# Kernel optimization log

Measured on AMD Instinct MI355X. Metric: run time of the kernel, lower is better.

The kernel has to match this reference:

```python
import jax, jax.numpy as jnp
import numpy as np

NUM_CLASSES = 100
CLUSTERS_PER_CLASS = 64
LATENT_DIM = 128
BATCH = 32768


def setup_inputs() -> dict:
    key = jax.random.key(0)
    kx, kc, kl = jax.random.split(key, 3)
    x = jax.random.normal(kx, (BATCH, LATENT_DIM), dtype=jnp.float32)
    # nn.Parameter(torch.randn(C, Kc, D) * 0.1)
    centers = jax.random.normal(kc, (NUM_CLASSES, CLUSTERS_PER_CLASS, LATENT_DIM), dtype=jnp.float32) * 0.1
    labels = jax.random.randint(kl, (BATCH,), 0, NUM_CLASSES, dtype=jnp.int64)
    return {"x": x, "centers": centers, "labels": labels}


def reference(x, centers, labels):
    # [C, Kc, D] -> [K, D]
    all_centers = centers.reshape(-1, LATENT_DIM).astype(x.dtype)
    x2 = jnp.sum(x * x, axis=-1, keepdims=True)            # [B,1]
    c2 = jnp.sum(all_centers * all_centers, axis=-1)       # [K]
    sq = x2 + c2[None, :] - 2.0 * jnp.einsum('bd,kd->bk', x, all_centers)
    distances = jnp.sqrt(jnp.maximum(sq, 0.0))             # [B,K]
    closest_indices = jnp.argmin(distances, axis=1)        # [B]
    class_predictions = closest_indices // CLUSTERS_PER_CLASS
    cluster_assignments = closest_indices % CLUSTERS_PER_CLASS
    quantized_hard = all_centers[closest_indices]          # [B,D]
    min_distances = jnp.take_along_axis(distances, closest_indices[:, None], axis=1)[:, 0]
    # straight-through estimator (training path in the torch module)
    quantized = x + jax.lax.stop_gradient(quantized_hard - x)
    return quantized, cluster_assignments, min_distances, class_predictions
```

## Files before the change

### kernel.cpp

```cpp
#include <hip/hip_runtime.h>
#include <math.h>

#define BATCH  32768
#define D      128
#define K      6400
#define KC     64
#define ROWS_PER_BLOCK 64
#define CHUNK_C 128
#define NCHUNKS 50

typedef _Float16 half8 __attribute__((ext_vector_type(8)));
typedef float    floatx4 __attribute__((ext_vector_type(4)));

typedef __attribute__((address_space(3))) unsigned       lds_uint;
typedef __attribute__((address_space(1))) const unsigned glb_uint;

__device__ __forceinline__ void async_lds16(const void* g, void* l) {
    __builtin_amdgcn_global_load_lds((glb_uint*)g, (lds_uint*)l, 16, 0, 0);
}

__global__ __launch_bounds__(256) void pack_kernel(const float* __restrict__ centers,
                                                   _Float16* __restrict__ wh,
                                                   float* __restrict__ c2n) {
    int tid = blockIdx.x * 256 + threadIdx.x;
    int ch = tid >> 11;
    int u  = (tid >> 7) & 15;
    int cw = tid & 127;
    int center = ch * CHUNK_C + cw;
    const float* src = centers + (size_t)center * D + u * 8;
    float4 a = *(const float4*)src;
    float4 b = *(const float4*)(src + 4);
    float f[8] = {a.x, a.y, a.z, a.w, b.x, b.y, b.z, b.w};
    half8 h;
#pragma unroll
    for (int j = 0; j < 8; ++j) h[j] = (_Float16)f[j];
    *(half8*)(wh + (size_t)tid * 8) = h;

    if (blockIdx.x < K / KC) {
        int c_local = threadIdx.x >> 2, part = threadIdx.x & 3;
        int c = blockIdx.x * 64 + c_local;
        const float4* p = (const float4*)(centers + (size_t)c * D + part * 32);
        float s = 0.f;
#pragma unroll
        for (int i = 0; i < 8; ++i) {
            float4 v = p[i];
            s = fmaf(v.x, v.x, s); s = fmaf(v.y, v.y, s);
            s = fmaf(v.z, v.z, s); s = fmaf(v.w, v.w, s);
        }
        s += __shfl_xor(s, 1, 64);
        s += __shfl_xor(s, 2, 64);
        if (part == 0) c2n[c] = -0.5f * s;
    }
}

__global__ __launch_bounds__(512, 4) void dist_kernel(
    const float* __restrict__ x, const float* __restrict__ centers,
    const _Float16* __restrict__ wh, const float* __restrict__ c2n,
    float* __restrict__ out) {
    __shared__ char lds[65536];

    const int t    = threadIdx.x;
    const int w    = t >> 6;
    const int L    = t & 63;
    const int quad = L >> 4;
    const int n16  = L & 15;
    const int cq   = w & 3;
    const int rq   = w >> 2;
    const int gr0  = blockIdx.x * ROWS_PER_BLOCK;

    half8 Ah[2][4];
#pragma unroll
    for (int rt = 0; rt < 2; ++rt) {
        int r = gr0 + rq * 32 + rt * 16 + n16;
        const float* xr = x + (size_t)r * D + quad * 8;
#pragma unroll
        for (int ks = 0; ks < 4; ++ks) {
            float4 a = *(const float4*)(xr + ks * 32);
            float4 b = *(const float4*)(xr + ks * 32 + 4);
            float f[8] = {a.x, a.y, a.z, a.w, b.x, b.y, b.z, b.w};
            half8 h;
#pragma unroll
            for (int j = 0; j < 8; ++j) h[j] = (_Float16)f[j];
            Ah[rt][ks] = h;
        }
    }

    float b1[8], b2[8];
#pragma unroll
    for (int k = 0; k < 8; ++k) { b1[k] = -1e30f; b2[k] = -1e30f; }

    const char* gh = (const char*)wh;

#pragma unroll
    for (int i = 0; i < 4; ++i) {
        int seg = w + i * 8;
        async_lds16(gh + seg * 1024 + L * 16, lds + seg * 1024);
    }

    float c2vA[2], c2vB[2];
#pragma unroll
    for (int ct = 0; ct < 2; ++ct) c2vA[ct] = c2n[cq * 32 + ct * 16 + n16];
    __syncthreads();

    for (int ci = 0; ci < NCHUNKS; ++ci) {
        const char* cur = lds + (ci & 1) * 32768;
        if (ci + 1 < NCHUNKS) {
            const char* gn = gh + (size_t)(ci + 1) * 32768;
            char* nxt = lds + ((ci + 1) & 1) * 32768;
#pragma unroll
            for (int i = 0; i < 4; ++i) {
                int seg = w + i * 8;
                async_lds16(gn + seg * 1024 + L * 16, nxt + seg * 1024);
            }
            const int kb1 = (ci + 1) * CHUNK_C + cq * 32;
#pragma unroll
            for (int ct = 0; ct < 2; ++ct) c2vB[ct] = c2n[kb1 + ct * 16 + n16];
        }

        floatx4 acc[2][2];
#pragma unroll
        for (int rt = 0; rt < 2; ++rt)
#pragma unroll
            for (int ct = 0; ct < 2; ++ct)
                acc[rt][ct] = (floatx4){c2vA[ct], c2vA[ct], c2vA[ct], c2vA[ct]};

        __builtin_amdgcn_s_setprio(1);
#pragma unroll
        for (int ks = 0; ks < 4; ++ks) {
            const half8* pb = (const half8*)cur + (ks * 4 + quad) * 128 + cq * 32 + n16;
#pragma unroll
            for (int ct = 0; ct < 2; ++ct) {
                half8 Bf = pb[ct * 16];
                acc[0][ct] = __builtin_amdgcn_mfma_f32_16x16x32_f16(Ah[0][ks], Bf, acc[0][ct], 0, 0, 0);
                acc[1][ct] = __builtin_amdgcn_mfma_f32_16x16x32_f16(Ah[1][ks], Bf, acc[1][ct], 0, 0, 0);
            }
        }
        __builtin_amdgcn_s_setprio(0);

        const unsigned pk0 = (unsigned)(2 * ci);
        const unsigned pk1 = (unsigned)(2 * ci + 1);
#pragma unroll
        for (int rt = 0; rt < 2; ++rt)
#pragma unroll
            for (int reg = 0; reg < 4; ++reg) {
                int k = rt * 4 + reg;
                float v0 = __uint_as_float((__float_as_uint(acc[rt][0][reg]) & ~127u) | pk0);
                float v1 = __uint_as_float((__float_as_uint(acc[rt][1][reg]) & ~127u) | pk1);
                float v  = fmaxf(v0, v1);
                b2[k] = __builtin_amdgcn_fmed3f(b1[k], b2[k], v);
                b1[k] = fmaxf(b1[k], v);
            }

#pragma unroll
        for (int ct = 0; ct < 2; ++ct) c2vA[ct] = c2vB[ct];

        __syncthreads();
    }

    int* candL = (int*)lds;

#pragma unroll
    for (int k = 0; k < 8; ++k) {
        unsigned u1 = __float_as_uint(b1[k]), u2 = __float_as_uint(b2[k]);
        int e1 = (int)(u1 & 127u), e2 = (int)(u2 & 127u);
        int p1 = (e1 >> 1) * 128 + cq * 32 + (e1 & 1) * 16 + n16;
        int p2 = (e2 >> 1) * 128 + cq * 32 + (e2 & 1) * 16 + n16;
        float v1 = b1[k], v2 = b2[k];
#pragma unroll
        for (int m = 1; m < 16; m <<= 1) {
            float o1 = __shfl_xor(v1, m, 64), o2 = __shfl_xor(v2, m, 64);
            int   q1 = __shfl_xor(p1, m, 64), q2 = __shfl_xor(p2, m, 64);
            bool firstMine = (v1 > o1) || (v1 == o1 && p1 < q1);
            float nv1 = firstMine ? v1 : o1;  int np1 = firstMine ? p1 : q1;
            float cb  = firstMine ? o1 : v1;  int cpi = firstMine ? q1 : p1;
            float ob  = firstMine ? v2 : o2;  int obi = firstMine ? p2 : q2;
            bool secOwn = (ob > cb) || (ob == cb && obi < cpi);
            v1 = nv1; p1 = np1;
            v2 = secOwn ? ob : cb;  p2 = secOwn ? obi : cpi;
        }
        if (n16 == 0) {
            int rloc = rq * 32 + (k >> 2) * 16 + quad * 4 + (k & 3);
            candL[rloc * 8 + cq * 2 + 0] = p1;
            candL[rloc * 8 + cq * 2 + 1] = p2;
        }
    }
    __syncthreads();

    {
        int r = t >> 3, p = t & 7;
        int row = gr0 + r;
        int ix = candL[r * 8 + p];
        const float4* xr4 = (const float4*)(x + (size_t)row * D);
        const float4* c4  = (const float4*)(centers + (size_t)ix * D);
        float dot = 0.f, x2s = 0.f, c2 = 0.f;
#pragma unroll
        for (int d4 = 0; d4 < 32; ++d4) {
            float4 xv = xr4[d4], cv = c4[d4];
            dot = fmaf(xv.x, cv.x, dot); dot = fmaf(xv.y, cv.y, dot);
            dot = fmaf(xv.z, cv.z, dot); dot = fmaf(xv.w, cv.w, dot);
            x2s = fmaf(xv.x, xv.x, x2s); x2s = fmaf(xv.y, xv.y, x2s);
            x2s = fmaf(xv.z, xv.z, x2s); x2s = fmaf(xv.w, xv.w, x2s);
            c2  = fmaf(cv.x, cv.x, c2);  c2  = fmaf(cv.y, cv.y, c2);
            c2  = fmaf(cv.z, cv.z, c2);  c2  = fmaf(cv.w, cv.w, c2);
        }
        float sq = x2s + c2 - 2.f * dot;
#pragma unroll
        for (int m = 1; m < 8; m <<= 1) {
            float osq = __shfl_xor(sq, m, 64);
            int   oix = __shfl_xor(ix, m, 64);
            if (osq < sq || (osq == sq && oix < ix)) { sq = osq; ix = oix; }
        }

        float* out_clu = out + (size_t)BATCH * D;
        float* out_md  = out_clu + BATCH;
        float* out_cls = out_md + BATCH;
        if (p == 0) {
            out_md[row]  = sqrtf(fmaxf(sq, 0.f));
            out_clu[row] = (float)(ix & (KC - 1));
            out_cls[row] = (float)(ix >> 6);
        }

        const float4* cv4 = (const float4*)(centers + (size_t)ix * D) + p * 4;
        const float4* xv4 = (const float4*)(x + (size_t)row * D) + p * 4;
        float4* o4 = (float4*)(out + (size_t)row * D) + p * 4;
#pragma unroll
        for (int i = 0; i < 4; ++i) {
            float4 cv = cv4[i], xv = xv4[i];
            float4 o;
            o.x = xv.x + (cv.x - xv.x);
            o.y = xv.y + (cv.y - xv.y);
            o.z = xv.z + (cv.z - xv.z);
            o.w = xv.w + (cv.w - xv.w);
            o4[i] = o;
        }
    }
}

extern "C" void kernel_launch(void* const* d_in, const int* in_sizes, int n_in,
                              void* d_out, int out_size, void* d_ws, size_t ws_size,
                              hipStream_t stream) {
    const float* x       = (const float*)d_in[0];
    const float* centers = (const float*)d_in[1];
    float* out = (float*)d_out;

    _Float16* wh  = (_Float16*)d_ws;
    float*    c2n = (float*)(wh + (size_t)K * D);

    pack_kernel<<<(K * 16) / 256, 256, 0, stream>>>(centers, wh, c2n);
    dist_kernel<<<BATCH / ROWS_PER_BLOCK, 512, 0, stream>>>(x, centers, wh, c2n, out);
}
```

Measured before the change: 174.5 us.

## Switch to triple-buffered 64-center chunks with one barrier per chunk

Halves the center chunk to 64 entries (16KB) and uses three LDS buffers, prefetching two chunks ahead. The loop now needs only a single s_barrier per chunk, gated by explicit vmcnt waits, and the packing layout and candidate index decode are updated to match. LDS per block drops, which allows raising the occupancy hint from 4 to 6 blocks per CU. In exchange there are twice as many chunk iterations and barriers, and less MFMA work between synchronisations.

Result: slower. 189.7 us (+8.7%).

```diff
diff --git a/kernel.cpp b/kernel.cpp
--- a/kernel.cpp
+++ b/kernel.cpp
@@ -6,8 +6,9 @@
 #define K      6400
 #define KC     64
 #define ROWS_PER_BLOCK 64
-#define CHUNK_C 128
-#define NCHUNKS 50
+#define CHUNK_C 64
+#define NCHUNKS 100
+#define CHUNK_BYTES 16384
 
 typedef _Float16 half8 __attribute__((ext_vector_type(8)));
 typedef float    floatx4 __attribute__((ext_vector_type(4)));
@@ -23,9 +24,9 @@
                                                    _Float16* __restrict__ wh,
                                                    float* __restrict__ c2n) {
     int tid = blockIdx.x * 256 + threadIdx.x;
-    int ch = tid >> 11;
-    int u  = (tid >> 7) & 15;
-    int cw = tid & 127;
+    int ch = tid >> 10;
+    int u  = (tid >> 6) & 15;
+    int cw = tid & 63;
     int center = ch * CHUNK_C + cw;
     const float* src = centers + (size_t)center * D + u * 8;
     float4 a = *(const float4*)src;
@@ -53,11 +54,12 @@
     }
 }
 
-__global__ __launch_bounds__(512, 4) void dist_kernel(
+__global__ __launch_bounds__(512, 6) void dist_kernel(
     const float* __restrict__ x, const float* __restrict__ centers,
     const _Float16* __restrict__ wh, const float* __restrict__ c2n,
     float* __restrict__ out) {
-    __shared__ char lds[65536];
+    __shared__ char bufs[3][CHUNK_BYTES];
+    __shared__ int  candL[ROWS_PER_BLOCK * 8];
 
     const int t    = threadIdx.x;
     const int w    = t >> 6;
@@ -90,81 +92,78 @@
     for (int k = 0; k < 8; ++k) { b1[k] = -1e30f; b2[k] = -1e30f; }
 
     const char* gh = (const char*)wh;
-
-#pragma unroll
-    for (int i = 0; i < 4; ++i) {
+    const int laneoff = cq * 16 + n16;
+
+    char* pA = bufs[0];  char* pB = bufs[1];  char* pC = bufs[2];
+#pragma unroll
+    for (int i = 0; i < 2; ++i) {
         int seg = w + i * 8;
-        async_lds16(gh + seg * 1024 + L * 16, lds + seg * 1024);
-    }
-
-    float c2vA[2], c2vB[2];
-#pragma unroll
-    for (int ct = 0; ct < 2; ++ct) c2vA[ct] = c2n[cq * 32 + ct * 16 + n16];
-    __syncthreads();
+        async_lds16(gh + seg * 1024 + L * 16, pA + seg * 1024);
+    }
+    float c2cur = c2n[laneoff];
+#pragma unroll
+    for (int i = 0; i < 2; ++i) {
+        int seg = w + i * 8;
+        async_lds16(gh + CHUNK_BYTES + seg * 1024 + L * 16, pB + seg * 1024);
+    }
+    float c2nxt = c2n[CHUNK_C + laneoff];
 
     for (int ci = 0; ci < NCHUNKS; ++ci) {
-        const char* cur = lds + (ci & 1) * 32768;
-        if (ci + 1 < NCHUNKS) {
-            const char* gn = gh + (size_t)(ci + 1) * 32768;
-            char* nxt = lds + ((ci + 1) & 1) * 32768;
-#pragma unroll
-            for (int i = 0; i < 4; ++i) {
+        if (ci + 1 < NCHUNKS) { asm volatile("s_waitcnt vmcnt(3)" ::: "memory"); }
+        else                  { asm volatile("s_waitcnt vmcnt(0)" ::: "memory"); }
+        __builtin_amdgcn_sched_barrier(0);
+        __builtin_amdgcn_s_barrier();
+        __builtin_amdgcn_sched_barrier(0);
+
+        floatx4 cinit = (floatx4){c2cur, c2cur, c2cur, c2cur};
+        const half8* pb = (const half8*)pA + quad * 64 + laneoff;
+        floatx4 acc0, acc1;
+        __builtin_amdgcn_s_setprio(1);
+        {
+            half8 Bf = pb[0];
+            acc0 = __builtin_amdgcn_mfma_f32_16x16x32_f16(Ah[0][0], Bf, cinit, 0, 0, 0);
+            acc1 = __builtin_amdgcn_mfma_f32_16x16x32_f16(Ah[1][0], Bf, cinit, 0, 0, 0);
+        }
+#pragma unroll
+        for (int ks = 1; ks < 4; ++ks) {
+            half8 Bf = pb[ks * 256];
+            acc0 = __builtin_amdgcn_mfma_f32_16x16x32_f16(Ah[0][ks], Bf, acc0, 0, 0, 0);
+            acc1 = __builtin_amdgcn_mfma_f32_16x16x32_f16(Ah[1][ks], Bf, acc1, 0, 0, 0);
+        }
+        __builtin_amdgcn_s_setprio(0);
+
+        float c2new = 0.f;
+        if (ci + 2 < NCHUNKS) {
+            const char* gn = gh + (size_t)(ci + 2) * CHUNK_BYTES;
+#pragma unroll
+            for (int i = 0; i < 2; ++i) {
                 int seg = w + i * 8;
-                async_lds16(gn + seg * 1024 + L * 16, nxt + seg * 1024);
+                async_lds16(gn + seg * 1024 + L * 16, pC + seg * 1024);
             }
-            const int kb1 = (ci + 1) * CHUNK_C + cq * 32;
-#pragma unroll
-            for (int ct = 0; ct < 2; ++ct) c2vB[ct] = c2n[kb1 + ct * 16 + n16];
-        }
-
-        floatx4 acc[2][2];
-#pragma unroll
-        for (int rt = 0; rt < 2; ++rt)
-#pragma unroll
-            for (int ct = 0; ct < 2; ++ct)
-                acc[rt][ct] = (floatx4){c2vA[ct], c2vA[ct], c2vA[ct], c2vA[ct]};
-
-        __builtin_amdgcn_s_setprio(1);
-#pragma unroll
-        for (int ks = 0; ks < 4; ++ks) {
-            const half8* pb = (const half8*)cur + (ks * 4 + quad) * 128 + cq * 32 + n16;
-#pragma unroll
-            for (int ct = 0; ct < 2; ++ct) {
-                half8 Bf = pb[ct * 16];
-                acc[0][ct] = __builtin_amdgcn_mfma_f32_16x16x32_f16(Ah[0][ks], Bf, acc[0][ct], 0, 0, 0);
-                acc[1][ct] = __builtin_amdgcn_mfma_f32_16x16x32_f16(Ah[1][ks], Bf, acc[1][ct], 0, 0, 0);
-            }
-        }
-        __builtin_amdgcn_s_setprio(0);
-
-        const unsigned pk0 = (unsigned)(2 * ci);
-        const unsigned pk1 = (unsigned)(2 * ci + 1);
-#pragma unroll
-        for (int rt = 0; rt < 2; ++rt)
-#pragma unroll
-            for (int reg = 0; reg < 4; ++reg) {
-                int k = rt * 4 + reg;
-                float v0 = __uint_as_float((__float_as_uint(acc[rt][0][reg]) & ~127u) | pk0);
-                float v1 = __uint_as_float((__float_as_uint(acc[rt][1][reg]) & ~127u) | pk1);
-                float v  = fmaxf(v0, v1);
-                b2[k] = __builtin_amdgcn_fmed3f(b1[k], b2[k], v);
-                b1[k] = fmaxf(b1[k], v);
-            }
-
-#pragma unroll
-        for (int ct = 0; ct < 2; ++ct) c2vA[ct] = c2vB[ct];
-
-        __syncthreads();
-    }
-
-    int* candL = (int*)lds;
+            c2new = c2n[(ci + 2) * CHUNK_C + laneoff];
+        }
+        c2cur = c2nxt; c2nxt = c2new;
+
+        const unsigned pk = (unsigned)ci;
+#pragma unroll
+        for (int reg = 0; reg < 4; ++reg) {
+            float v0 = __uint_as_float((__float_as_uint(acc0[reg]) & ~127u) | pk);
+            b2[reg] = __builtin_amdgcn_fmed3f(b1[reg], b2[reg], v0);
+            b1[reg] = fmaxf(b1[reg], v0);
+            float v1 = __uint_as_float((__float_as_uint(acc1[reg]) & ~127u) | pk);
+            b2[4 + reg] = __builtin_amdgcn_fmed3f(b1[4 + reg], b2[4 + reg], v1);
+            b1[4 + reg] = fmaxf(b1[4 + reg], v1);
+        }
+
+        char* tmp = pA; pA = pB; pB = pC; pC = tmp;
+    }
 
 #pragma unroll
     for (int k = 0; k < 8; ++k) {
         unsigned u1 = __float_as_uint(b1[k]), u2 = __float_as_uint(b2[k]);
         int e1 = (int)(u1 & 127u), e2 = (int)(u2 & 127u);
-        int p1 = (e1 >> 1) * 128 + cq * 32 + (e1 & 1) * 16 + n16;
-        int p2 = (e2 >> 1) * 128 + cq * 32 + (e2 & 1) * 16 + n16;
+        int p1 = e1 * CHUNK_C + laneoff;
+        int p2 = e2 * CHUNK_C + laneoff;
         float v1 = b1[k], v2 = b2[k];
 #pragma unroll
         for (int m = 1; m < 16; m <<= 1) {
```
